# Kernel tuning notes

Hardware: AMD Instinct MI355X
Metric: run time of the kernel (lower is better)

## Reference

```python
import jax, jax.numpy as jnp
import numpy as np

NUM_CLASSES = 10
BATCH = 2048
DIM = 128
TEMPERATURE = 0.07
BASE_TEMPERATURE = 0.07


def setup_inputs() -> dict:
    key = jax.random.key(0)
    k1, k2 = jax.random.split(key)
    preds = jax.random.normal(k1, (NUM_CLASSES, BATCH, DIM), dtype=jnp.float32)
    target = jax.random.randint(k2, (BATCH,), 0, NUM_CLASSES, dtype=jnp.int64)
    log_vars = jnp.zeros((NUM_CLASSES,), dtype=jnp.float32)
    return {"preds": preds, "target": target, "log_vars": log_vars}


def _per_class_loss(features, labels_bin):
    # features: [B, D], labels_bin: [B] in {0,1} (target == class i)
    B = features.shape[0]
    mask = (labels_bin[:, None] == labels_bin[None, :]).astype(features.dtype)  # [B,B]
    logits_mask = 1.0 - jnp.eye(B, dtype=features.dtype)                        # zero diagonal
    sim = jnp.matmul(features, features.T) / TEMPERATURE                        # [B,B]
    norms = jnp.linalg.norm(features, axis=1, keepdims=True)                    # [B,1]
    logits = sim / (norms * norms.T)                                            # cosine / temp
    mask = mask * logits_mask
    exp_logits = jnp.exp(logits) * logits_mask
    log_prob = logits - jnp.log(exp_logits.sum(axis=1, keepdims=True))
    mean_log_prob_pos = (mask * log_prob).sum(axis=1) / mask.sum(axis=1)
    loss = -(TEMPERATURE / BASE_TEMPERATURE) * mean_log_prob_pos
    return loss.mean()


def reference(preds, target, log_vars):
    # labels_bin[i] = (target == i), one row per class
    labels_bin = (target[None, :] == jnp.arange(NUM_CLASSES, dtype=target.dtype)[:, None])
    losses = jax.vmap(_per_class_loss)(preds, labels_bin)  # [num_classes]
    final_loss = jnp.sum(jnp.exp(-log_vars) * losses + log_vars)
    return final_loss
```

## Files before the change

### kernel.cpp

```cpp
#include <hip/hip_runtime.h>
#include <hip/hip_bf16.h>
#include <math.h>

#define NUM_CLASSES 10
#define BATCH 2048
#define DIM 128
#define INV_T 14.285714285714286f
#define NTILE 16
#define NPAIR 136

typedef __attribute__((ext_vector_type(8))) short bf16x8;
typedef __attribute__((ext_vector_type(4))) float f32x4;

__device__ __forceinline__ void load_lds16(const void* g, void* lds) {
    __builtin_amdgcn_global_load_lds(
        (const __attribute__((address_space(1))) unsigned int*)g,
        (__attribute__((address_space(3))) unsigned int*)lds,
        16, 0, 0);
}

__global__ __launch_bounds__(256) void normalize_kernel(
    const float* __restrict__ preds, __hip_bfloat16* __restrict__ g,
    const float* __restrict__ log_vars, float* __restrict__ out)
{
    int b = blockIdx.x;
    int t = threadIdx.x;
    if (b == 0 && t == 0) {
        float lv = 0.0f;
        for (int i = 0; i < NUM_CLASSES; ++i) lv += log_vars[i];
        out[0] = lv;
    }

    int row  = b * 4 + (t >> 6);
    int lane = t & 63;
    const float2* src = (const float2*)(preds + (size_t)row * DIM);
    float2 v = src[lane];
    float ss = v.x * v.x + v.y * v.y;
#pragma unroll
    for (int m = 32; m; m >>= 1) ss += __shfl_xor(ss, m, 64);
    float rn = 1.0f / sqrtf(ss);
    __hip_bfloat162 o;
    o.x = __float2bfloat16(v.x * rn);
    o.y = __float2bfloat16(v.y * rn);
    *(__hip_bfloat162*)(g + (size_t)row * DIM + lane * 2) = o;
}

__global__ __launch_bounds__(256) void gram_kernel(
    const __hip_bfloat16* __restrict__ g, const int* __restrict__ target,
    float2* __restrict__ part)
{
    int p = blockIdx.x;
    int by = 0, rem = NTILE;
    while (p >= rem) { p -= rem; --rem; ++by; }
    const int bx   = by + p;
    const int cls  = blockIdx.y;
    const int row0 = by * 128;
    const int col0 = bx * 128;
    const bool isDiag = (by == bx);
    const ushort* gc = (const ushort*)g + (size_t)cls * BATCH * DIM;

    __shared__ __align__(16) ushort smem[2 * 128 * 128];
    __shared__ int tgt[256];
    ushort* As = smem;
    ushort* Bs = smem + 128 * 128;

    const int t    = threadIdx.x;
    const int wid  = t >> 6;
    const int lane = t & 63;
    const int tx   = lane & 15;
    const int quad = lane >> 4;
    const int wm   = (wid >> 1) * 64;
    const int wn   = (wid & 1) * 64;

    tgt[t] = (t < 128) ? target[row0 + t] : target[col0 + (t - 128)];

    const int lr = lane >> 4;
    const int lp = lane & 15;
#pragma unroll
    for (int s = 0; s < 8; ++s) {
        int rb = s * 16 + wid * 4;
        int r  = rb + lr;
        int c  = lp ^ (r & 15);
        load_lds16(gc + (size_t)(row0 + r) * DIM + c * 8, &As[rb * 128]);
        if (!isDiag)
            load_lds16(gc + (size_t)(col0 + r) * DIM + c * 8, &Bs[rb * 128]);
    }
    __syncthreads();

    const ushort* BsR = isDiag ? As : Bs;
    f32x4 acc[4][4] = {};
#pragma unroll
    for (int ks = 0; ks < 4; ++ks) {
        bf16x8 af[4], bg[4];
#pragma unroll
        for (int i = 0; i < 4; ++i) {
            int pa = ((ks * 4 + quad) ^ tx) * 8;
            af[i] = *(const bf16x8*)&As [(wm + i * 16 + tx) * 128 + pa];
            bg[i] = *(const bf16x8*)&BsR[(wn + i * 16 + tx) * 128 + pa];
        }
#pragma unroll
        for (int i = 0; i < 4; ++i)
#pragma unroll
            for (int j = 0; j < 4; ++j)
                acc[i][j] = __builtin_amdgcn_mfma_f32_16x16x32_bf16(
                    af[i], bg[j], acc[i][j], 0, 0, 0);
    }
    __syncthreads();

    unsigned laMask = 0;
#pragma unroll
    for (int i = 0; i < 4; ++i)
#pragma unroll
        for (int r = 0; r < 4; ++r)
            if (tgt[wm + i * 16 + quad * 4 + r] == cls)
                laMask |= 1u << (i * 4 + r);
    int lb[4];
#pragma unroll
    for (int j = 0; j < 4; ++j) lb[j] = (tgt[128 + wn + j * 16 + tx] == cls);

    float2* rbuf = (float2*)smem;
    float2* cbuf = (float2*)(smem + 17408);
    float2 pcol[4] = {};

#pragma unroll
    for (int i = 0; i < 4; ++i) {
        float2 prow[4] = {};
#pragma unroll
        for (int j = 0; j < 4; ++j) {
            int cg = col0 + wn + j * 16 + tx;
            int lbj = lb[j];
#pragma unroll
            for (int r = 0; r < 4; ++r) {
                int rg = row0 + wm + i * 16 + quad * 4 + r;
                float logit = acc[i][j][r] * INV_T;
                float e = __expf(logit);
                bool dg = isDiag && (cg == rg);
                e = dg ? 0.0f : e;
                bool same = (((laMask >> (i * 4 + r)) & 1) == (unsigned)lbj) && !dg;
                float sl = same ? logit : 0.0f;
                prow[r].x += e; prow[r].y += sl;
                pcol[j].x += e; pcol[j].y += sl;
            }
        }
#pragma unroll
        for (int r = 0; r < 4; ++r)
            rbuf[wid * 1088 + (i * 16 + quad * 4 + r) * 17 + tx] = prow[r];
    }
#pragma unroll
    for (int j = 0; j < 4; ++j)
        cbuf[wid * 320 + (j * 16 + tx) * 5 + quad] = pcol[j];
    __syncthreads();

    if (t < 128) {
        int rl = t & 63, grp = t >> 6;
        float den = 0.0f, sp = 0.0f;
#pragma unroll
        for (int w = 0; w < 2; ++w) {
            int base = (2 * grp + w) * 1088 + rl * 17;
#pragma unroll
            for (int x = 0; x < 16; ++x) {
                float2 v = rbuf[base + x];
                den += v.x; sp += v.y;
            }
        }
        part[((size_t)(cls * NTILE + bx)) * BATCH + row0 + t] = make_float2(den, sp);
    } else if (!isDiag) {
        int u = t - 128;
        int cl = u & 63, grp = u >> 6;
        float den = 0.0f, sp = 0.0f;
#pragma unroll
        for (int w = 0; w < 2; ++w) {
            int base = (grp + 2 * w) * 320 + cl * 5;
#pragma unroll
            for (int q = 0; q < 4; ++q) {
                float2 v = cbuf[base + q];
                den += v.x; sp += v.y;
            }
        }
        part[((size_t)(cls * NTILE + by)) * BATCH + col0 + u] = make_float2(den, sp);
    }
}

__global__ __launch_bounds__(256) void final_kernel(
    const float2* __restrict__ part, const int* __restrict__ target,
    const float* __restrict__ log_vars, float* __restrict__ out)
{
    __shared__ int cw[4];
    __shared__ float wred[4];
    const int t   = threadIdx.x;
    const int idx = blockIdx.x * 256 + t;
    const int cls = idx >> 11;
    const int a   = idx & (BATCH - 1);

    int c = 0;
#pragma unroll
    for (int k = 0; k < 8; ++k) c += (target[t * 8 + k] == cls);
#pragma unroll
    for (int m = 1; m < 64; m <<= 1) c += __shfl_xor(c, m, 64);
    if ((t & 63) == 0) cw[t >> 6] = c;
    __syncthreads();
    const int c1 = cw[0] + cw[1] + cw[2] + cw[3];

    float den = 0.0f, sp = 0.0f;
#pragma unroll
    for (int s = 0; s < NTILE; ++s) {
        float2 v = part[((size_t)(cls * NTILE + s)) * BATCH + a];
        den += v.x; sp += v.y;
    }

    const int la  = (target[a] == cls);
    const int cnt = la ? (c1 - 1) : (BATCH - c1 - 1);
    float mlpp = sp / (float)cnt - logf(den);
    float prt = __expf(-log_vars[cls]) * mlpp;
#pragma unroll
    for (int m = 32; m; m >>= 1) prt += __shfl_xor(prt, m, 64);
    if ((t & 63) == 0) wred[t >> 6] = prt;
    __syncthreads();
    if (t == 0)
        atomicAdd(out, -(wred[0] + wred[1] + wred[2] + wred[3]) / (float)BATCH);
}

extern "C" void kernel_launch(void* const* d_in, const int* in_sizes, int n_in,
                              void* d_out, int out_size, void* d_ws, size_t ws_size,
                              hipStream_t stream)
{
    const float* preds    = (const float*)d_in[0];
    const int*   target   = (const int*)  d_in[1];
    const float* log_vars = (const float*)d_in[2];
    float* out = (float*)d_out;

    __hip_bfloat16* gbf = (__hip_bfloat16*)d_ws;
    float2* part = (float2*)((char*)d_ws +
                             (size_t)NUM_CLASSES * BATCH * DIM * 2);

    normalize_kernel<<<NUM_CLASSES * BATCH / 4, 256, 0, stream>>>(
        preds, gbf, log_vars, out);
    gram_kernel<<<dim3(NPAIR, NUM_CLASSES), 256, 0, stream>>>(gbf, target, part);
    final_kernel<<<NUM_CLASSES * BATCH / 256, 256, 0, stream>>>(
        part, target, log_vars, out);
}
```

Measured before the change: 86.88 us.

## Fuse final reduction into gram kernel via last-block atomic counter

Removes the separate final kernel launch: each gram block increments a per-class atomic counter, and the last block for a class reduces that class's partials and adds its loss to the output. The epilogue now uses exp2f with a prescaled constant, and is specialized for diagonal versus off-diagonal tiles so the diagonal check compiles out for most blocks. The tail reduction runs on only one block per class, so its parallelism is reduced, and the change relies on the counter being zeroed by the normalize kernel.

```diff
diff --git a/kernel.cpp b/kernel.cpp
--- a/kernel.cpp
+++ b/kernel.cpp
@@ -6,6 +6,7 @@
 #define BATCH 2048
 #define DIM 128
 #define INV_T 14.285714285714286f
+#define SCALE 20.60992915555662f
 #define NTILE 16
 #define NPAIR 136
 
@@ -21,14 +22,18 @@
 
 __global__ __launch_bounds__(256) void normalize_kernel(
     const float* __restrict__ preds, __hip_bfloat16* __restrict__ g,
-    const float* __restrict__ log_vars, float* __restrict__ out)
+    const float* __restrict__ log_vars, float* __restrict__ out,
+    int* __restrict__ cnt)
 {
     int b = blockIdx.x;
     int t = threadIdx.x;
-    if (b == 0 && t == 0) {
-        float lv = 0.0f;
-        for (int i = 0; i < NUM_CLASSES; ++i) lv += log_vars[i];
-        out[0] = lv;
+    if (b == 0) {
+        if (t < NUM_CLASSES) cnt[t] = 0;
+        if (t == 0) {
+            float lv = 0.0f;
+            for (int i = 0; i < NUM_CLASSES; ++i) lv += log_vars[i];
+            out[0] = lv;
+        }
     }
 
     int row  = b * 4 + (t >> 6);
@@ -47,7 +52,8 @@
 
 __global__ __launch_bounds__(256) void gram_kernel(
     const __hip_bfloat16* __restrict__ g, const int* __restrict__ target,
-    float2* __restrict__ part)
+    float2* __restrict__ part, int* __restrict__ cnt,
+    const float* __restrict__ log_vars, float* __restrict__ out)
 {
     int p = blockIdx.x;
     int by = 0, rem = NTILE;
@@ -61,6 +67,9 @@
 
     __shared__ __align__(16) ushort smem[2 * 128 * 128];
     __shared__ int tgt[256];
+    __shared__ int lastFlag;
+    __shared__ int cw[4];
+    __shared__ float wred[4];
     ushort* As = smem;
     ushort* Bs = smem + 128 * 128;
 
@@ -122,30 +131,35 @@
     float2* cbuf = (float2*)(smem + 17408);
     float2 pcol[4] = {};
 
-#pragma unroll
-    for (int i = 0; i < 4; ++i) {
-        float2 prow[4] = {};
-#pragma unroll
-        for (int j = 0; j < 4; ++j) {
-            int cg = col0 + wn + j * 16 + tx;
-            int lbj = lb[j];
-#pragma unroll
-            for (int r = 0; r < 4; ++r) {
-                int rg = row0 + wm + i * 16 + quad * 4 + r;
-                float logit = acc[i][j][r] * INV_T;
-                float e = __expf(logit);
-                bool dg = isDiag && (cg == rg);
-                e = dg ? 0.0f : e;
-                bool same = (((laMask >> (i * 4 + r)) & 1) == (unsigned)lbj) && !dg;
-                float sl = same ? logit : 0.0f;
-                prow[r].x += e; prow[r].y += sl;
-                pcol[j].x += e; pcol[j].y += sl;
-            }
-        }
-#pragma unroll
-        for (int r = 0; r < 4; ++r)
-            rbuf[wid * 1088 + (i * 16 + quad * 4 + r) * 17 + tx] = prow[r];
-    }
+#define EPILOGUE(DIAG)                                                         \
+    _Pragma("unroll")                                                          \
+    for (int i = 0; i < 4; ++i) {                                              \
+        float2 prow[4] = {};                                                   \
+        _Pragma("unroll")                                                      \
+        for (int j = 0; j < 4; ++j) {                                          \
+            int lbj = lb[j];                                                   \
+            _Pragma("unroll")                                                  \
+            for (int r = 0; r < 4; ++r) {                                      \
+                float a0 = acc[i][j][r];                                       \
+                float e = exp2f(a0 * SCALE);                                   \
+                bool dg = DIAG &&                                              \
+                    ((wn + j * 16 + tx) == (wm + i * 16 + quad * 4 + r));      \
+                e = dg ? 0.0f : e;                                             \
+                bool same = (((laMask >> (i * 4 + r)) & 1) == (unsigned)lbj)   \
+                            && !dg;                                            \
+                float sl = same ? a0 : 0.0f;                                   \
+                prow[r].x += e; prow[r].y += sl;                               \
+                pcol[j].x += e; pcol[j].y += sl;                               \
+            }                                                                  \
+        }                                                                      \
+        _Pragma("unroll")                                                      \
+        for (int r = 0; r < 4; ++r)                                           \
+            rbuf[wid * 1088 + (i * 16 + quad * 4 + r) * 17 + tx] = prow[r];    \
+    }
+
+    if (isDiag) { EPILOGUE(true) } else { EPILOGUE(false) }
+#undef EPILOGUE
+
 #pragma unroll
     for (int j = 0; j < 4; ++j)
         cbuf[wid * 320 + (j * 16 + tx) * 5 + quad] = pcol[j];
@@ -179,18 +193,16 @@
         }
         part[((size_t)(cls * NTILE + by)) * BATCH + col0 + u] = make_float2(den, sp);
     }
-}
-
-__global__ __launch_bounds__(256) void final_kernel(
-    const float2* __restrict__ part, const int* __restrict__ target,
-    const float* __restrict__ log_vars, float* __restrict__ out)
-{
-    __shared__ int cw[4];
-    __shared__ float wred[4];
-    const int t   = threadIdx.x;
-    const int idx = blockIdx.x * 256 + t;
-    const int cls = idx >> 11;
-    const int a   = idx & (BATCH - 1);
+
+    __threadfence();
+    __syncthreads();
+    if (t == 0) {
+        int old = atomicAdd(&cnt[cls], 1);
+        lastFlag = (old == NPAIR - 1);
+    }
+    __syncthreads();
+    if (!lastFlag) return;
+    __threadfence();
 
     int c = 0;
 #pragma unroll
@@ -201,23 +213,29 @@
     __syncthreads();
     const int c1 = cw[0] + cw[1] + cw[2] + cw[3];
 
-    float den = 0.0f, sp = 0.0f;
-#pragma unroll
-    for (int s = 0; s < NTILE; ++s) {
-        float2 v = part[((size_t)(cls * NTILE + s)) * BATCH + a];
-        den += v.x; sp += v.y;
-    }
-
-    const int la  = (target[a] == cls);
-    const int cnt = la ? (c1 - 1) : (BATCH - c1 - 1);
-    float mlpp = sp / (float)cnt - logf(den);
-    float prt = __expf(-log_vars[cls]) * mlpp;
-#pragma unroll
-    for (int m = 32; m; m >>= 1) prt += __shfl_xor(prt, m, 64);
-    if ((t & 63) == 0) wred[t >> 6] = prt;
-    __syncthreads();
-    if (t == 0)
-        atomicAdd(out, -(wred[0] + wred[1] + wred[2] + wred[3]) / (float)BATCH);
+    float accv = 0.0f;
+    const float2* pc = part + (size_t)cls * NTILE * BATCH;
+#pragma unroll
+    for (int k = 0; k < 8; ++k) {
+        int a = k * 256 + t;
+        float den = 0.0f, sp = 0.0f;
+#pragma unroll
+        for (int s = 0; s < NTILE; ++s) {
+            float2 v = pc[s * BATCH + a];
+            den += v.x; sp += v.y;
+        }
+        int la   = (target[a] == cls);
+        int ccnt = la ? (c1 - 1) : (BATCH - c1 - 1);
+        accv += (INV_T * sp) / (float)ccnt - logf(den);
+    }
+#pragma unroll
+    for (int m = 32; m; m >>= 1) accv += __shfl_xor(accv, m, 64);
+    if ((t & 63) == 0) wred[t >> 6] = accv;
+    __syncthreads();
+    if (t == 0) {
+        float s = wred[0] + wred[1] + wred[2] + wred[3];
+        atomicAdd(out, -__expf(-log_vars[cls]) * s / (float)BATCH);
+    }
 }
 
 extern "C" void kernel_launch(void* const* d_in, const int* in_sizes, int n_in,
@@ -229,13 +247,15 @@
     const float* log_vars = (const float*)d_in[2];
     float* out = (float*)d_out;
 
-    __hip_bfloat16* gbf = (__hip_bfloat16*)d_ws;
-    float2* part = (float2*)((char*)d_ws +
-                             (size_t)NUM_CLASSES * BATCH * DIM * 2);
+    char* ws = (char*)d_ws;
+    __hip_bfloat16* gbf = (__hip_bfloat16*)ws;
+    ws += (size_t)NUM_CLASSES * BATCH * DIM * 2;
+    float2* part = (float2*)ws;
+    ws += (size_t)NUM_CLASSES * NTILE * BATCH * sizeof(float2);
+    int* cnt = (int*)ws;
 
     normalize_kernel<<<NUM_CLASSES * BATCH / 4, 256, 0, stream>>>(
-        preds, gbf, log_vars, out);
-    gram_kernel<<<dim3(NPAIR, NUM_CLASSES), 256, 0, stream>>>(gbf, target, part);
-    final_kernel<<<NUM_CLASSES * BATCH / 256, 256, 0, stream>>>(
-        part, target, log_vars, out);
-}
+        preds, gbf, log_vars, out, cnt);
+    gram_kernel<<<dim3(NPAIR, NUM_CLASSES), 256, 0, stream>>>(
+        gbf, target, part, cnt, log_vars, out);
+}
```

Measured after the change: 200.8 us. +131.1%, slower.
